# Kernel optimization log

Measured on AMD Instinct MI355X. Metric: run time of the kernel, lower is better.

Reference implementation:

```python
import jax, jax.numpy as jnp
import numpy as np

TEMP = 0.3
LAM = 0.9
NUM_LABELS = 7
B, D = 8192, 768


def setup_inputs() -> dict:
    key = jax.random.key(0)
    k1, k2, k3, k4 = jax.random.split(key, 4)
    cls_emb = jax.random.normal(k1, (B, D), dtype=jnp.float32)
    pooled = jax.random.normal(k2, (B, D), dtype=jnp.float32)
    labels = jax.random.randint(k3, (B,), 0, NUM_LABELS)
    W = jax.random.normal(k4, (NUM_LABELS, D), dtype=jnp.float32) * 0.02
    b = jnp.zeros((NUM_LABELS,), dtype=jnp.float32)
    return {"cls_emb": cls_emb, "pooled": pooled, "labels": labels, "W": W, "b": b}


def reference(cls_emb, pooled, labels, W, b):
    # classifier head (dropout = identity in eval)
    logits = pooled @ W.T + b  # [B, num_labels]

    # cross-entropy (mean reduction, as nn.CrossEntropyLoss default)
    logp = jax.nn.log_softmax(logits, axis=-1)
    ce = -jnp.mean(jnp.take_along_axis(logp, labels[:, None], axis=1)[:, 0])

    # supervised contrastive loss on DETACHED cls embeddings (original uses .detach().numpy())
    e = jax.lax.stop_gradient(cls_emb)
    en = e / jnp.linalg.norm(e, axis=1, keepdims=True)
    S = (en @ en.T) / TEMP  # [B, B] scaled cosine similarity
    n = S.shape[0]
    eye = jnp.eye(n, dtype=bool)
    # row_sum excludes the diagonal -> stable off-diagonal logsumexp
    lse = jax.nn.logsumexp(jnp.where(eye, -jnp.inf, S), axis=1)  # [B]
    pos = (labels[:, None] == labels[None, :]) & ~eye  # [B, B]
    n_i = jnp.sum(pos, axis=1).astype(S.dtype)  # positives per anchor
    inner = jnp.sum(jnp.where(pos, S - lse[:, None], 0.0), axis=1)  # sum log(exp(s)/row_sum)
    per_anchor = jnp.where(n_i > 0, -inner / jnp.maximum(n_i, 1.0), 0.0)
    contrastive = jnp.sum(per_anchor)  # summed over anchors, as in original

    loss = LAM * contrastive + (1.0 - LAM) * ce
    return loss, logits
```

## Files before the change

kernel.cpp:

```cpp
#include <hip/hip_runtime.h>
#include <hip/hip_bf16.h>


#define B_N 8192
#define D_K 768
#define NLAB 7
#define MBOUND 3.3333333333333335f
#define RTINV 1.8257418583505538f

typedef float f32x4 __attribute__((ext_vector_type(4)));
typedef int i32x8 __attribute__((ext_vector_type(8)));

__device__ __forceinline__ void gl2lds16(const void* g, void* l) {
  __builtin_amdgcn_global_load_lds(
      (const __attribute__((address_space(1))) void*)g,
      (__attribute__((address_space(3))) void*)l, 16, 0, 0);
}

__device__ __forceinline__ float bf16u_to_f(unsigned short u) {
  return __uint_as_float(((unsigned int)u) << 16);
}

__device__ __forceinline__ float dec8(unsigned int b) {
  unsigned int s = (b >> 7) & 1u, e = (b >> 3) & 15u, m = b & 7u;
  float fn = __uint_as_float((s << 31) | ((e + 120u) << 23) | (m << 20));
  float fs = (s ? -1.f : 1.f) * (float)m * 0.001953125f;
  return e ? fn : fs;
}

template <int WBF>
__global__ __launch_bounds__(256) void k_prep(
    const float* __restrict__ cls, const float* __restrict__ pooled,
    const int* __restrict__ labels, const float* __restrict__ W,
    const float* __restrict__ bias, unsigned char* __restrict__ e8,
    unsigned short* __restrict__ en, float* __restrict__ logits_out,
    float* __restrict__ celoss, int* __restrict__ zr) {
  if (blockIdx.x == 0)
    for (int t = threadIdx.x; t < 9280; t += 256) zr[t] = 0;

  int wv = threadIdx.x >> 6, lane = threadIdx.x & 63;
  int row = blockIdx.x * 4 + wv;

  const float4* src = (const float4*)(cls + (size_t)row * D_K);
  float4 x[3];
  float ss = 0.f;
#pragma unroll
  for (int j = 0; j < 3; ++j) {
    x[j] = src[j * 64 + lane];
    ss += x[j].x * x[j].x + x[j].y * x[j].y + x[j].z * x[j].z + x[j].w * x[j].w;
  }
#pragma unroll
  for (int m = 1; m < 64; m <<= 1) ss += __shfl_xor(ss, m);
  float sc = rsqrtf(ss) * RTINV;
  int* d8 = (int*)(e8 + (size_t)row * D_K);
  ushort4* db = (ushort4*)(en + (size_t)row * D_K);
#pragma unroll
  for (int j = 0; j < 3; ++j) {
    int w32 = __builtin_amdgcn_cvt_pk_fp8_f32(x[j].x * sc, x[j].y * sc, 0, false);
    w32 = __builtin_amdgcn_cvt_pk_fp8_f32(x[j].z * sc, x[j].w * sc, w32, true);
    d8[j * 64 + lane] = w32;
    if (WBF) {
      const float* xv = reinterpret_cast<const float*>(&x[j]);
      ushort4 o;
      unsigned short* ov = reinterpret_cast<unsigned short*>(&o);
#pragma unroll
      for (int k = 0; k < 4; ++k) {
        __hip_bfloat16 h = __float2bfloat16(xv[k] * sc);
        ov[k] = *reinterpret_cast<unsigned short*>(&h);
      }
      db[j * 64 + lane] = o;
    }
  }

  const float4* p4 = (const float4*)(pooled + (size_t)row * D_K);
  float acc[NLAB];
#pragma unroll
  for (int c = 0; c < NLAB; ++c) acc[c] = 0.f;
#pragma unroll
  for (int j = 0; j < 3; ++j) {
    float4 xx = p4[j * 64 + lane];
#pragma unroll
    for (int c = 0; c < NLAB; ++c) {
      float4 w = ((const float4*)(W + c * D_K))[j * 64 + lane];
      acc[c] += xx.x * w.x + xx.y * w.y + xx.z * w.z + xx.w * w.w;
    }
  }
#pragma unroll
  for (int c = 0; c < NLAB; ++c)
#pragma unroll
    for (int m = 1; m < 64; m <<= 1) acc[c] += __shfl_xor(acc[c], m);
  if (lane == 0) {
    float l[NLAB], mx = -1e30f;
#pragma unroll
    for (int c = 0; c < NLAB; ++c) { l[c] = acc[c] + bias[c]; mx = fmaxf(mx, l[c]); }
    float se = 0.f;
#pragma unroll
    for (int c = 0; c < NLAB; ++c) se += __expf(l[c] - mx);
    float lse = mx + __logf(se);
    celoss[row] = lse - l[labels[row]];
    float* o = logits_out + (size_t)row * NLAB;
#pragma unroll
    for (int c = 0; c < NLAB; ++c) o[c] = l[c];
  }
}

template <int M>
__global__ __launch_bounds__(256) void k_classumA(
    const unsigned short* __restrict__ en, const unsigned char* __restrict__ e8,
    const int* __restrict__ labels, float* __restrict__ partial,
    int* __restrict__ hist) {
  int g = blockIdx.x, t = threadIdx.x;
  int slab = g >> 1, half = g & 1;
  int r0 = slab * 128;
  int dbase = half * 384;
  if (t < 96) {
    float acc[NLAB][4];
#pragma unroll
    for (int c = 0; c < NLAB; ++c)
#pragma unroll
      for (int k = 0; k < 4; ++k) acc[c][k] = 0.f;
    for (int r = 0; r < 128; r += 4) {
      int lab[4];
      float xv[4][4];
#pragma unroll
      for (int q = 0; q < 4; ++q) {
        int row = r0 + r + q;
        lab[q] = labels[row];
        if (M == 0) {
          ushort4 u = *(const ushort4*)(en + (size_t)row * D_K + dbase + t * 4);
          xv[q][0] = bf16u_to_f(u.x); xv[q][1] = bf16u_to_f(u.y);
          xv[q][2] = bf16u_to_f(u.z); xv[q][3] = bf16u_to_f(u.w);
        } else {
          uchar4 u = *(const uchar4*)(e8 + (size_t)row * D_K + dbase + t * 4);
          xv[q][0] = dec8(u.x); xv[q][1] = dec8(u.y);
          xv[q][2] = dec8(u.z); xv[q][3] = dec8(u.w);
        }
      }
#pragma unroll
      for (int q = 0; q < 4; ++q)
#pragma unroll
        for (int c = 0; c < NLAB; ++c) {
          bool m = (lab[q] == c);
          acc[c][0] += m ? xv[q][0] : 0.f;
          acc[c][1] += m ? xv[q][1] : 0.f;
          acc[c][2] += m ? xv[q][2] : 0.f;
          acc[c][3] += m ? xv[q][3] : 0.f;
        }
    }
    float* dst = partial + (size_t)slab * (NLAB * D_K) + dbase;
#pragma unroll
    for (int c = 0; c < NLAB; ++c) {
      float4 v = {acc[c][0], acc[c][1], acc[c][2], acc[c][3]};
      *(float4*)(dst + c * D_K + t * 4) = v;
    }
  } else if (t >= 192 && half == 0) {
    int lane = t - 192;
    int cnt[NLAB];
#pragma unroll
    for (int c = 0; c < NLAB; ++c) cnt[c] = 0;
#pragma unroll
    for (int q = 0; q < 2; ++q) {
      int lab = labels[r0 + q * 64 + lane];
#pragma unroll
      for (int c = 0; c < NLAB; ++c) cnt[c] += (lab == c);
    }
#pragma unroll
    for (int c = 0; c < NLAB; ++c)
#pragma unroll
      for (int m = 1; m < 64; m <<= 1) cnt[c] += __shfl_xor(cnt[c], m);
    if (lane == 0)
#pragma unroll
      for (int c = 0; c < NLAB; ++c) atomicAdd(&hist[c], cnt[c]);
  }
}

__global__ __launch_bounds__(256) void k_scl(const unsigned char* __restrict__ e8,
                                             float* __restrict__ rse,
                                             const float* __restrict__ partial,
                                             float* __restrict__ T) {
  if (blockIdx.x >= 2080) {
    int idx = (int)(blockIdx.x - 2080) * 256 + threadIdx.x;
    float v = 0.f;
    for (int g = 0; g < 64; ++g) v += partial[(size_t)g * (NLAB * D_K) + idx];
    T[idx] = v;
    return;
  }
  __shared__ __align__(16) unsigned char As[2][128 * 128];
  __shared__ __align__(16) unsigned char Bs[2][128 * 128];

  int rem = blockIdx.x;
  int BI = 0, BJ = 0;
  for (;;) {
    int sz = (BI == BJ) ? 36 : 64;
    if (rem < sz) break;
    rem -= sz;
    if (++BJ == 8) { ++BI; BJ = BI; }
  }
  int bi, bj;
  if (BI == BJ) {
    int r = 0, w = 8;
    while (rem >= w) { rem -= w; ++r; --w; }
    bi = BI * 8 + r;
    bj = BJ * 8 + r + rem;
  } else {
    bi = BI * 8 + (rem >> 3);
    bj = BJ * 8 + (rem & 7);
  }

  const int i0 = bi * 128, j0 = bj * 128;
  const int tid = threadIdx.x, wv = tid >> 6, lane = tid & 63;
  const int quad = lane >> 4, cix = lane & 15;
  const int rowTile = 64 * (wv >> 1), colTile = 64 * (wv & 1);

  int aoff[4], boff[4], lbase[4];
#pragma unroll
  for (int it = 0; it < 4; ++it) {
    int s = it * 256 + tid;
    int r = s >> 3;
    int p = ((s & 7) - r) & 7;
    aoff[it] = (i0 + r) * D_K + p * 16;
    boff[it] = (j0 + r) * D_K + p * 16;
    lbase[it] = (it * 256 + wv * 64) * 16;
  }

  f32x4 acc[4][4] = {};

#pragma unroll
  for (int it = 0; it < 4; ++it) {
    gl2lds16(e8 + (size_t)aoff[it], (char*)As[0] + lbase[it]);
    gl2lds16(e8 + (size_t)boff[it], (char*)Bs[0] + lbase[it]);
  }

#pragma unroll
  for (int kc = 0; kc < 6; ++kc) {
    const int cb = kc & 1;
    __builtin_amdgcn_sched_barrier(0);
    asm volatile("s_waitcnt vmcnt(0)" ::: "memory");
    __builtin_amdgcn_s_barrier();
    asm volatile("" ::: "memory");
    if (kc < 5) {
#pragma unroll
      for (int it = 0; it < 4; ++it) {
        gl2lds16(e8 + (size_t)(aoff[it] + (kc + 1) * 128), (char*)As[cb ^ 1] + lbase[it]);
        gl2lds16(e8 + (size_t)(boff[it] + (kc + 1) * 128), (char*)Bs[cb ^ 1] + lbase[it]);
      }
    }
    asm volatile("" ::: "memory");
    i32x8 aF[4];
#pragma unroll
    for (int mt = 0; mt < 4; ++mt) {
      int r = rowTile + 16 * mt + cix;
      const char* base = (const char*)As[cb] + r * 128;
      int4 lo = *(const int4*)(base + (((quad * 2 + 0) + r) & 7) * 16);
      int4 hi = *(const int4*)(base + (((quad * 2 + 1) + r) & 7) * 16);
      aF[mt][0] = lo.x; aF[mt][1] = lo.y; aF[mt][2] = lo.z; aF[mt][3] = lo.w;
      aF[mt][4] = hi.x; aF[mt][5] = hi.y; aF[mt][6] = hi.z; aF[mt][7] = hi.w;
    }
#pragma unroll
    for (int nt = 0; nt < 4; ++nt) {
      int r = colTile + 16 * nt + cix;
      const char* base = (const char*)Bs[cb] + r * 128;
      int4 lo = *(const int4*)(base + (((quad * 2 + 0) + r) & 7) * 16);
      int4 hi = *(const int4*)(base + (((quad * 2 + 1) + r) & 7) * 16);
      i32x8 bF;
      bF[0] = lo.x; bF[1] = lo.y; bF[2] = lo.z; bF[3] = lo.w;
      bF[4] = hi.x; bF[5] = hi.y; bF[6] = hi.z; bF[7] = hi.w;
#pragma unroll
      for (int mt = 0; mt < 4; ++mt)
        acc[mt][nt] = __builtin_amdgcn_mfma_scale_f32_16x16x128_f8f6f4(
            aF[mt], bF, acc[mt][nt], 0, 0, 0, 127, 0, 127);
    }
  }

  if (bi != bj) {
    float ce_col[4] = {0.f, 0.f, 0.f, 0.f};
#pragma unroll
    for (int mt = 0; mt < 4; ++mt) {
      int rowbase = i0 + rowTile + 16 * mt + quad * 4;
      float rs_e[4] = {0.f, 0.f, 0.f, 0.f};
#pragma unroll
      for (int nt = 0; nt < 4; ++nt) {
#pragma unroll
        for (int rg = 0; rg < 4; ++rg) {
          float e = __expf(acc[mt][nt][rg] - MBOUND);
          rs_e[rg] += e;
          ce_col[nt] += e;
        }
      }
#pragma unroll
      for (int rg = 0; rg < 4; ++rg)
#pragma unroll
        for (int m = 1; m <= 8; m <<= 1) rs_e[rg] += __shfl_xor(rs_e[rg], m);
      if (cix == 0)
#pragma unroll
        for (int rg = 0; rg < 4; ++rg) atomicAdd(&rse[rowbase + rg], rs_e[rg]);
    }
#pragma unroll
    for (int nt = 0; nt < 4; ++nt) {
      ce_col[nt] += __shfl_xor(ce_col[nt], 16);
      ce_col[nt] += __shfl_xor(ce_col[nt], 32);
    }
    if (quad == 0)
#pragma unroll
      for (int nt = 0; nt < 4; ++nt)
        atomicAdd(&rse[j0 + colTile + 16 * nt + cix], ce_col[nt]);
  } else {
#pragma unroll
    for (int mt = 0; mt < 4; ++mt) {
      int rowbase = i0 + rowTile + 16 * mt + quad * 4;
      float rs_e[4] = {0.f, 0.f, 0.f, 0.f};
#pragma unroll
      for (int nt = 0; nt < 4; ++nt) {
        int gcol = j0 + colTile + 16 * nt + cix;
#pragma unroll
        for (int rg = 0; rg < 4; ++rg) {
          bool dg = (rowbase + rg) == gcol;
          rs_e[rg] += dg ? 0.f : __expf(acc[mt][nt][rg] - MBOUND);
        }
      }
#pragma unroll
      for (int rg = 0; rg < 4; ++rg)
#pragma unroll
        for (int m = 1; m <= 8; m <<= 1) rs_e[rg] += __shfl_xor(rs_e[rg], m);
      if (cix == 0)
#pragma unroll
        for (int rg = 0; rg < 4; ++rg) atomicAdd(&rse[rowbase + rg], rs_e[rg]);
    }
  }
}

template <int M>
__global__ __launch_bounds__(256) void k_rowfinal(
    const float* __restrict__ rse, const unsigned short* __restrict__ en,
    const unsigned char* __restrict__ e8, const float* __restrict__ T,
    const int* __restrict__ labels, const int* __restrict__ hist,
    const float* __restrict__ celoss, float* __restrict__ contrP,
    int* __restrict__ done_count, float* __restrict__ out) {
  __shared__ float part[4];
  int wv = threadIdx.x >> 6, lane = threadIdx.x & 63;
  int row = blockIdx.x * 4 + wv;
  int l = labels[row];
  const float4* t4 = (const float4*)(T + (size_t)l * D_K);
  float pd = 0.f, sd = 0.f;
#pragma unroll
  for (int j = 0; j < 3; ++j) {
    float a0, a1, a2, a3;
    if (M == 0) {
      ushort4 u = ((const ushort4*)(en + (size_t)row * D_K))[j * 64 + lane];
      a0 = bf16u_to_f(u.x); a1 = bf16u_to_f(u.y);
      a2 = bf16u_to_f(u.z); a3 = bf16u_to_f(u.w);
    } else {
      uint u = ((const uint*)(e8 + (size_t)row * D_K))[j * 64 + lane];
      a0 = dec8(u & 0xff); a1 = dec8((u >> 8) & 0xff);
      a2 = dec8((u >> 16) & 0xff); a3 = dec8(u >> 24);
    }
    float4 t = t4[j * 64 + lane];
    pd += a0 * t.x + a1 * t.y + a2 * t.z + a3 * t.w;
    sd += a0 * a0 + a1 * a1 + a2 * a2 + a3 * a3;
  }
#pragma unroll
  for (int m = 1; m < 64; m <<= 1) {
    pd += __shfl_xor(pd, m);
    sd += __shfl_xor(sd, m);
  }
  if (lane == 0) {
    int ni = hist[l] - 1;
    float per = 0.f;
    if (ni > 0) per = MBOUND + __logf(rse[row]) - (pd - sd) / (float)ni;
    part[wv] = 0.9f * per + (0.1f / (float)B_N) * celoss[row];
  }
  __syncthreads();
  if (threadIdx.x == 0) {
    float v = part[0] + part[1] + part[2] + part[3];
    atomicAdd(&contrP[(blockIdx.x & 63) * 16], v);
    __threadfence();
    int n = atomicAdd(done_count, 1);
    if (n == (int)gridDim.x - 1) {
      float s = 0.f;
      for (int i = 0; i < 64; ++i)
        s += __hip_atomic_load(&contrP[i * 16], __ATOMIC_RELAXED,
                               __HIP_MEMORY_SCOPE_AGENT);
      out[0] = s;
    }
  }
}

extern "C" void kernel_launch(void* const* d_in, const int* in_sizes, int n_in,
                              void* d_out, int out_size, void* d_ws, size_t ws_size,
                              hipStream_t stream) {
  const float* cls    = (const float*)d_in[0];
  const float* pooled = (const float*)d_in[1];
  const int*   labels = (const int*)d_in[2];
  const float* W      = (const float*)d_in[3];
  const float* bias   = (const float*)d_in[4];
  float* out = (float*)d_out;

  char* ws = (char*)d_ws;
  unsigned char* e8 = (unsigned char*)ws;
  const size_t EN_B = (size_t)B_N * D_K * 2;
  const size_t E8_B = (size_t)B_N * D_K;
  size_t need_big = E8_B + EN_B + 98304 + 64 * (size_t)(NLAB * D_K) * 4;
  bool big = ws_size >= need_big;
  unsigned short* en = (unsigned short*)(ws + E8_B);
  size_t off = big ? (E8_B + EN_B) : E8_B;
  float* rse     = (float*)(ws + off);
  int*   hist    = (int*)(ws + off + 32768);
  int*   done    = (int*)(ws + off + 32896);
  float* contrP  = (float*)(ws + off + 33024);
  float* T       = (float*)(ws + off + 37120);
  float* celoss  = (float*)(ws + off + 58624);
  float* partial = (float*)(ws + off + 98304);
  int*   zr      = (int*)(ws + off);

  if (big)
    k_prep<1><<<B_N / 4, 256, 0, stream>>>(cls, pooled, labels, W, bias, e8, en,
                                           out + 1, celoss, zr);
  else
    k_prep<0><<<B_N / 4, 256, 0, stream>>>(cls, pooled, labels, W, bias, e8, en,
                                           out + 1, celoss, zr);
  if (big)
    k_classumA<0><<<128, 256, 0, stream>>>(en, e8, labels, partial, hist);
  else
    k_classumA<1><<<128, 256, 0, stream>>>(en, e8, labels, partial, hist);
  k_scl<<<2101, 256, 0, stream>>>(e8, rse, partial, T);
  if (big)
    k_rowfinal<0><<<B_N / 4, 256, 0, stream>>>(rse, en, e8, T, labels, hist,
                                               celoss, contrP, done, out);
  else
    k_rowfinal<1><<<B_N / 4, 256, 0, stream>>>(rse, en, e8, T, labels, hist,
                                               celoss, contrP, done, out);
}
```

Before: 225.3 us.

## Load MFMA fragments directly from global memory instead of LDS staging

Removes the double-buffered LDS staging (global_load_lds into As/Bs, with barriers and waits) in the FP8 similarity GEMM kernel. Each wave now reads its A and B fragments straight from global memory. This drops the LDS traffic and the workgroup barriers, and frees LDS, which may allow higher occupancy. The cost is that operand reuse across waves now depends on L1/L2 caches instead of shared memory, and the loads are no longer prefetched ahead of the MFMAs.

Measured after the change: 290.0 us. 1.29x slower.

```diff
diff --git a/kernel.cpp b/kernel.cpp
--- a/kernel.cpp
+++ b/kernel.cpp
@@ -10,12 +10,6 @@
 
 typedef float f32x4 __attribute__((ext_vector_type(4)));
 typedef int i32x8 __attribute__((ext_vector_type(8)));
-
-__device__ __forceinline__ void gl2lds16(const void* g, void* l) {
-  __builtin_amdgcn_global_load_lds(
-      (const __attribute__((address_space(1))) void*)g,
-      (__attribute__((address_space(3))) void*)l, 16, 0, 0);
-}
 
 __device__ __forceinline__ float bf16u_to_f(unsigned short u) {
   return __uint_as_float(((unsigned int)u) << 16);
@@ -185,8 +179,6 @@
     T[idx] = v;
     return;
   }
-  __shared__ __align__(16) unsigned char As[2][128 * 128];
-  __shared__ __align__(16) unsigned char Bs[2][128 * 128];
 
   int rem = blockIdx.x;
   int BI = 0, BJ = 0;
@@ -212,56 +204,30 @@
   const int quad = lane >> 4, cix = lane & 15;
   const int rowTile = 64 * (wv >> 1), colTile = 64 * (wv & 1);
 
-  int aoff[4], boff[4], lbase[4];
-#pragma unroll
-  for (int it = 0; it < 4; ++it) {
-    int s = it * 256 + tid;
-    int r = s >> 3;
-    int p = ((s & 7) - r) & 7;
-    aoff[it] = (i0 + r) * D_K + p * 16;
-    boff[it] = (j0 + r) * D_K + p * 16;
-    lbase[it] = (it * 256 + wv * 64) * 16;
+  const unsigned char* arow[4];
+  const unsigned char* brow[4];
+#pragma unroll
+  for (int mt = 0; mt < 4; ++mt) {
+    arow[mt] = e8 + (size_t)(i0 + rowTile + 16 * mt + cix) * D_K + quad * 32;
+    brow[mt] = e8 + (size_t)(j0 + colTile + 16 * mt + cix) * D_K + quad * 32;
   }
 
   f32x4 acc[4][4] = {};
 
 #pragma unroll
-  for (int it = 0; it < 4; ++it) {
-    gl2lds16(e8 + (size_t)aoff[it], (char*)As[0] + lbase[it]);
-    gl2lds16(e8 + (size_t)boff[it], (char*)Bs[0] + lbase[it]);
-  }
-
-#pragma unroll
   for (int kc = 0; kc < 6; ++kc) {
-    const int cb = kc & 1;
-    __builtin_amdgcn_sched_barrier(0);
-    asm volatile("s_waitcnt vmcnt(0)" ::: "memory");
-    __builtin_amdgcn_s_barrier();
-    asm volatile("" ::: "memory");
-    if (kc < 5) {
-#pragma unroll
-      for (int it = 0; it < 4; ++it) {
-        gl2lds16(e8 + (size_t)(aoff[it] + (kc + 1) * 128), (char*)As[cb ^ 1] + lbase[it]);
-        gl2lds16(e8 + (size_t)(boff[it] + (kc + 1) * 128), (char*)Bs[cb ^ 1] + lbase[it]);
-      }
-    }
-    asm volatile("" ::: "memory");
     i32x8 aF[4];
 #pragma unroll
     for (int mt = 0; mt < 4; ++mt) {
-      int r = rowTile + 16 * mt + cix;
-      const char* base = (const char*)As[cb] + r * 128;
-      int4 lo = *(const int4*)(base + (((quad * 2 + 0) + r) & 7) * 16);
-      int4 hi = *(const int4*)(base + (((quad * 2 + 1) + r) & 7) * 16);
+      int4 lo = *(const int4*)(arow[mt] + kc * 128);
+      int4 hi = *(const int4*)(arow[mt] + kc * 128 + 16);
       aF[mt][0] = lo.x; aF[mt][1] = lo.y; aF[mt][2] = lo.z; aF[mt][3] = lo.w;
       aF[mt][4] = hi.x; aF[mt][5] = hi.y; aF[mt][6] = hi.z; aF[mt][7] = hi.w;
     }
 #pragma unroll
     for (int nt = 0; nt < 4; ++nt) {
-      int r = colTile + 16 * nt + cix;
-      const char* base = (const char*)Bs[cb] + r * 128;
-      int4 lo = *(const int4*)(base + (((quad * 2 + 0) + r) & 7) * 16);
-      int4 hi = *(const int4*)(base + (((quad * 2 + 1) + r) & 7) * 16);
+      int4 lo = *(const int4*)(brow[nt] + kc * 128);
+      int4 hi = *(const int4*)(brow[nt] + kc * 128 + 16);
       i32x8 bF;
       bF[0] = lo.x; bF[1] = lo.y; bF[2] = lo.z; bF[3] = lo.w;
       bF[4] = hi.x; bF[5] = hi.y; bF[6] = hi.z; bF[7] = hi.w;
```
